# Kernel optimization log

Hardware: AMD Instinct MI355X
Metric: run time of the kernel (lower is better)

The kernel has to match this reference:

```python
import jax, jax.numpy as jnp
import numpy as np
from jax import lax

B, CIN, H, W = 1, 1024, 48, 160
FEAT = 64            # PSM_features
D = 48               # depth_channel = max_disp / downsample_scale
EPS = 1e-5


def _bn(x, g, b, m, v, ndim):
    # eval-mode batchnorm over channel axis 1
    shape = (1, -1) + (1,) * (ndim - 2)
    return (x - m.reshape(shape)) * (g.reshape(shape) * lax.rsqrt(v.reshape(shape) + EPS)) + b.reshape(shape)


def _conv3d(x, w, b):
    y = lax.conv_general_dilated(x, w, (1, 1, 1), 'SAME',
                                 dimension_numbers=('NCDHW', 'OIDHW', 'NCDHW'))
    return y + b[None, :, None, None, None]


def setup_inputs() -> dict:
    key = jax.random.key(0)
    ks = jax.random.split(key, 24)
    f32 = jnp.float32
    inp = {}
    inp['left_features'] = jax.random.normal(ks[0], (B, CIN, H, W), f32)
    inp['right_features'] = jax.random.normal(ks[1], (B, CIN, H, W), f32)
    # 1x1 down_sample conv + BN2d
    inp['ds_w'] = jax.random.normal(ks[2], (FEAT, CIN), f32) * (1.0 / np.sqrt(CIN))
    inp['ds_b'] = jax.random.normal(ks[3], (FEAT,), f32) * 0.01
    inp['bn2_g'] = jax.random.uniform(ks[4], (FEAT,), f32, 0.9, 1.1)
    inp['bn2_b'] = jax.random.normal(ks[5], (FEAT,), f32) * 0.01
    inp['bn2_m'] = jax.random.normal(ks[6], (FEAT,), f32) * 0.01
    inp['bn2_v'] = jax.random.uniform(ks[7], (FEAT,), f32, 0.5, 1.5)
    # conv3d block 1: 2*FEAT -> FEAT, 3x3x3
    inp['c3a_w'] = jax.random.normal(ks[8], (FEAT, 2 * FEAT, 3, 3, 3), f32) * (1.0 / np.sqrt(2 * FEAT * 27))
    inp['c3a_b'] = jax.random.normal(ks[9], (FEAT,), f32) * 0.01
    inp['bn3a_g'] = jax.random.uniform(ks[10], (FEAT,), f32, 0.9, 1.1)
    inp['bn3a_b'] = jax.random.normal(ks[11], (FEAT,), f32) * 0.01
    inp['bn3a_m'] = jax.random.normal(ks[12], (FEAT,), f32) * 0.01
    inp['bn3a_v'] = jax.random.uniform(ks[13], (FEAT,), f32, 0.5, 1.5)
    # conv3d block 2: FEAT -> FEAT, 3x3x3
    inp['c3b_w'] = jax.random.normal(ks[14], (FEAT, FEAT, 3, 3, 3), f32) * (1.0 / np.sqrt(FEAT * 27))
    inp['c3b_b'] = jax.random.normal(ks[15], (FEAT,), f32) * 0.01
    inp['bn3b_g'] = jax.random.uniform(ks[16], (FEAT,), f32, 0.9, 1.1)
    inp['bn3b_b'] = jax.random.normal(ks[17], (FEAT,), f32) * 0.01
    inp['bn3b_m'] = jax.random.normal(ks[18], (FEAT,), f32) * 0.01
    inp['bn3b_v'] = jax.random.uniform(ks[19], (FEAT,), f32, 0.5, 1.5)
    return inp


def reference(left_features, right_features, ds_w, ds_b, bn2_g, bn2_b, bn2_m, bn2_v,
              c3a_w, c3a_b, bn3a_g, bn3a_b, bn3a_m, bn3a_v,
              c3b_w, c3b_b, bn3b_g, bn3b_b, bn3b_m, bn3b_v):
    def down_sample(x):
        y = jnp.einsum('bchw,oc->bohw', x, ds_w) + ds_b[None, :, None, None]
        return jax.nn.relu(_bn(y, bn2_g, bn2_b, bn2_m, bn2_v, 4))

    left = down_sample(left_features)    # [B,FEAT,H,W]
    right = down_sample(right_features)  # [B,FEAT,H,W]

    # Cost volume: for disparity i, left copied at w>=i, right shifted right by i.
    d_idx = jnp.arange(D)[:, None]        # [D,1]
    w_idx = jnp.arange(W)[None, :]        # [1,W]
    mask = (w_idx >= d_idx).astype(left.dtype)          # [D,W]
    cost_left = left[:, :, None, :, :] * mask[None, None, :, None, :]  # [B,F,D,H,W]
    shift = jnp.clip(w_idx - d_idx, 0, W - 1)           # [D,W], right[..., w-i]
    right_g = right[:, :, :, shift]                     # [B,F,H,D,W]
    cost_right = jnp.transpose(right_g, (0, 1, 3, 2, 4)) * mask[None, None, :, None, :]
    cost = jnp.concatenate([cost_left, cost_right], axis=1)  # [B,2F,D,H,W]

    y = jax.nn.relu(_bn(_conv3d(cost, c3a_w, c3a_b), bn3a_g, bn3a_b, bn3a_m, bn3a_v, 5))
    y = jax.nn.relu(_bn(_conv3d(y, c3b_w, c3b_b), bn3b_g, bn3b_b, bn3b_m, bn3b_v, 5))
    return y.reshape(B, -1, H, W)  # [B, FEAT*D, H, W]
```

## Files before the change

### kernel.cpp

```cpp
#include <hip/hip_runtime.h>
#include <hip/hip_bf16.h>

#define CIN   1024
#define FEATN 64
#define HH    48
#define WW    160
#define DDN   48
#define EPSV  1e-5f
#define NTAP  27
#define WSLAB 162

typedef __attribute__((ext_vector_type(8))) short bf16x8;
typedef __attribute__((ext_vector_type(4))) float f32x4;
typedef __attribute__((ext_vector_type(4))) unsigned short u16x4;

static __device__ __forceinline__ unsigned short f2bf(float x) {
    __hip_bfloat16 h = __float2bfloat16(x);
    return *(unsigned short*)&h;
}

__global__ void CostVolume_6201932775918_packw(const float* w3, unsigned short* Wb)
{
    int i = (int)(blockIdx.x * 256 + threadIdx.x);
    if (i >= 64 * NTAP * 128) return;
    int ci  = i & 127;
    int tap = (i >> 7) % NTAP;
    int o   = i / (NTAP * 128);
    Wb[i] = f2bf(w3[o * 3456 + ci * 27 + tap]);
}

__global__ void CostVolume_6201932775918_packw2(const float* w3, unsigned short* Wb2)
{
    int i = (int)(blockIdx.x * 256 + threadIdx.x);
    if (i >= 64 * NTAP * 64) return;
    int ci  = i & 63;
    int tap = (i >> 6) % NTAP;
    int o   = i / (NTAP * 64);
    Wb2[i] = f2bf(w3[o * 1728 + ci * 27 + tap]);
}

__global__ void CostVolume_6201932775918_ds(
    const float* Lf, const float* Rf,
    const float* dsw, const float* dsb,
    const float* g2, const float* b2, const float* m2, const float* v2,
    unsigned short* outL, unsigned short* outR)
{
    const float* in = (blockIdx.y == 0) ? Lf : Rf;
    unsigned short* out = (blockIdx.y == 0) ? outL : outR;
    const int t    = (int)threadIdx.x;
    const int pos0 = (int)blockIdx.x * 64;
    const int oq   = t & 15;
    const int pq   = t >> 4;

    __shared__ float chunk[64 * 64];

    float acc[4][4];
    #pragma unroll
    for (int k = 0; k < 4; ++k)
        #pragma unroll
        for (int j = 0; j < 4; ++j) acc[k][j] = 0.f;

    for (int cc = 0; cc < 16; ++cc) {
        __syncthreads();
        #pragma unroll
        for (int i = 0; i < 16; ++i) {
            int idx = i * 256 + t;
            int cl = idx >> 6;
            int p  = idx & 63;
            chunk[cl * 64 + p] = in[(cc * 64 + cl) * (HH * WW) + pos0 + p];
        }
        __syncthreads();
        for (int cl = 0; cl < 64; ++cl) {
            int c = cc * 64 + cl;
            float x0 = chunk[cl * 64 + pq * 4 + 0];
            float x1 = chunk[cl * 64 + pq * 4 + 1];
            float x2 = chunk[cl * 64 + pq * 4 + 2];
            float x3 = chunk[cl * 64 + pq * 4 + 3];
            #pragma unroll
            for (int k = 0; k < 4; ++k) {
                float w = dsw[(4 * oq + k) * CIN + c];
                acc[k][0] = fmaf(w, x0, acc[k][0]);
                acc[k][1] = fmaf(w, x1, acc[k][1]);
                acc[k][2] = fmaf(w, x2, acc[k][2]);
                acc[k][3] = fmaf(w, x3, acc[k][3]);
            }
        }
    }

    float s4[4], cb4[4];
    #pragma unroll
    for (int k = 0; k < 4; ++k) {
        int o = 4 * oq + k;
        s4[k]  = g2[o] / sqrtf(v2[o] + EPSV);
        cb4[k] = dsb[o] * s4[k] + b2[o] - m2[o] * s4[k];
    }
    #pragma unroll
    for (int j = 0; j < 4; ++j) {
        u16x4 v;
        #pragma unroll
        for (int k = 0; k < 4; ++k)
            v[k] = f2bf(fmaxf(0.f, fmaf(acc[k][j], s4[k], cb4[k])));
        *(u16x4*)&out[(size_t)(pos0 + pq * 4 + j) * 64 + 4 * oq] = v;
    }
}

__global__ __launch_bounds__(256) void CostVolume_6201932775918_c3a(
    const unsigned short* Lt, const unsigned short* Rt,
    const unsigned short* Wb,
    const float* cb3, const float* g3, const float* b3,
    const float* m3, const float* v3,
    unsigned short* y1t)
{
    const int h    = (int)blockIdx.x;
    const int d    = (int)blockIdx.y;
    const int t    = (int)threadIdx.x;
    const int wave = t >> 6;
    const int lane = t & 63;
    const int l15  = lane & 15;
    const int lhi  = lane >> 4;

    __shared__ __align__(16) unsigned short slab[WSLAB * 128];

    f32x4 acc[10];
    #pragma unroll
    for (int n = 0; n < 10; ++n) acc[n] = (f32x4){0.f, 0.f, 0.f, 0.f};

    char* slabB = (char*)slab;
    const int sw0 = t >> 4;

    for (int kd = 0; kd < 3; ++kd) {
        const int dp = d + kd - 1;
        if (dp < 0 || dp >= DDN) continue;
        for (int kh = 0; kh < 3; ++kh) {
            const int hp = h + kh - 1;
            if (hp < 0 || hp >= HH) continue;
            __syncthreads();
            const unsigned short* Lrow = Lt + (size_t)hp * WW * 64;
            const unsigned short* Rrow = Rt + ((size_t)hp * WW - (size_t)dp) * 64;
            #pragma unroll
            for (int i = 0; i < 11; ++i) {
                int e = i * 256 + t;
                if (e < WSLAB * 16) {
                    int wIdx = e >> 4;
                    int c16  = e & 15;
                    int wp   = wIdx - 1;
                    u16x4 v0 = (u16x4){0, 0, 0, 0}, v1 = (u16x4){0, 0, 0, 0};
                    if (wp >= dp && wp < WW) {
                        const unsigned short* src =
                            (c16 < 8) ? (Lrow + (size_t)wp * 64 + c16 * 8)
                                      : (Rrow + (size_t)wp * 64 + (c16 - 8) * 8);
                        v0 = *(const u16x4*)src;
                        v1 = *(const u16x4*)(src + 4);
                    }
                    int byte = (wIdx * 256 + c16 * 16) ^ ((wIdx & 15) << 4);
                    *(u16x4*)(slabB + byte)     = v0;
                    *(u16x4*)(slabB + byte + 8) = v1;
                }
            }
            __syncthreads();
            const int tapbase = (kd * 3 + kh) * 3;
            #pragma unroll
            for (int kw = 0; kw < 3; ++kw) {
                const unsigned short* wrow =
                    Wb + (16 * wave + l15) * (NTAP * 128) + (tapbase + kw) * 128 + lhi * 8;
                #pragma unroll
                for (int kc = 0; kc < 4; ++kc) {
                    bf16x8 afrag = *(const bf16x8*)(wrow + kc * 32);
                    const int ci0x2 = (kc * 32 + lhi * 8) * 2;
                    #pragma unroll
                    for (int n = 0; n < 10; ++n) {
                        int wIdx = 16 * n + l15 + kw;
                        int byte = (wIdx * 256 + ci0x2) ^ ((wIdx & 15) << 4);
                        bf16x8 bfrag = *(const bf16x8*)(slabB + byte);
                        acc[n] = __builtin_amdgcn_mfma_f32_16x16x32_bf16(
                            afrag, bfrag, acc[n], 0, 0, 0);
                    }
                }
            }
        }
    }
    (void)sw0;

    float s4[4], cb4[4];
    #pragma unroll
    for (int r = 0; r < 4; ++r) {
        const int o = 16 * wave + lhi * 4 + r;
        s4[r]  = g3[o] / sqrtf(v3[o] + EPSV);
        cb4[r] = cb3[o] * s4[r] + b3[o] - m3[o] * s4[r];
    }
    unsigned short* ybase =
        y1t + ((size_t)(d * HH + h) * WW) * 64 + 16 * wave + lhi * 4;
    #pragma unroll
    for (int n = 0; n < 10; ++n) {
        int w = 16 * n + l15;
        u16x4 v;
        #pragma unroll
        for (int r = 0; r < 4; ++r)
            v[r] = f2bf(fmaxf(0.f, fmaf(acc[n][r], s4[r], cb4[r])));
        *(u16x4*)(ybase + (size_t)w * 64) = v;
    }
}

__global__ __launch_bounds__(256) void CostVolume_6201932775918_c3b(
    const unsigned short* y1t, const unsigned short* Wb2,
    const float* cb3, const float* g3, const float* b3,
    const float* m3, const float* v3,
    float* outp)
{
    const int h    = (int)blockIdx.x;
    const int d    = (int)blockIdx.y;
    const int t    = (int)threadIdx.x;
    const int wave = t >> 6;
    const int lane = t & 63;
    const int l15  = lane & 15;
    const int lhi  = lane >> 4;

    __shared__ __align__(16) unsigned short slab[WSLAB * 64];

    f32x4 acc[10];
    #pragma unroll
    for (int n = 0; n < 10; ++n) acc[n] = (f32x4){0.f, 0.f, 0.f, 0.f};

    char* slabB = (char*)slab;

    for (int kd = 0; kd < 3; ++kd) {
        const int dp = d + kd - 1;
        if (dp < 0 || dp >= DDN) continue;
        for (int kh = 0; kh < 3; ++kh) {
            const int hp = h + kh - 1;
            if (hp < 0 || hp >= HH) continue;
            __syncthreads();
            const unsigned short* yrow = y1t + ((size_t)(dp * HH + hp) * WW) * 64;
            #pragma unroll
            for (int i = 0; i < 6; ++i) {
                int e = i * 256 + t;
                if (e < WSLAB * 8) {
                    int wIdx = e >> 3;
                    int c16  = e & 7;
                    int wp   = wIdx - 1;
                    u16x4 v0 = (u16x4){0, 0, 0, 0}, v1 = (u16x4){0, 0, 0, 0};
                    if (wp >= 0 && wp < WW) {
                        const unsigned short* src = yrow + (size_t)wp * 64 + c16 * 8;
                        v0 = *(const u16x4*)src;
                        v1 = *(const u16x4*)(src + 4);
                    }
                    int byte = (wIdx * 128 + c16 * 16) ^ ((wIdx & 7) << 4);
                    *(u16x4*)(slabB + byte)     = v0;
                    *(u16x4*)(slabB + byte + 8) = v1;
                }
            }
            __syncthreads();
            const int tapbase = (kd * 3 + kh) * 3;
            #pragma unroll
            for (int kw = 0; kw < 3; ++kw) {
                const unsigned short* wrow =
                    Wb2 + (16 * wave + l15) * (NTAP * 64) + (tapbase + kw) * 64 + lhi * 8;
                #pragma unroll
                for (int kc = 0; kc < 2; ++kc) {
                    bf16x8 afrag = *(const bf16x8*)(wrow + kc * 32);
                    const int ci0x2 = (kc * 32 + lhi * 8) * 2;
                    #pragma unroll
                    for (int n = 0; n < 10; ++n) {
                        int wIdx = 16 * n + l15 + kw;
                        int byte = (wIdx * 128 + ci0x2) ^ ((wIdx & 7) << 4);
                        bf16x8 bfrag = *(const bf16x8*)(slabB + byte);
                        acc[n] = __builtin_amdgcn_mfma_f32_16x16x32_bf16(
                            afrag, bfrag, acc[n], 0, 0, 0);
                    }
                }
            }
        }
    }

    float s4[4], cb4[4];
    #pragma unroll
    for (int r = 0; r < 4; ++r) {
        const int o = 16 * wave + lhi * 4 + r;
        s4[r]  = g3[o] / sqrtf(v3[o] + EPSV);
        cb4[r] = cb3[o] * s4[r] + b3[o] - m3[o] * s4[r];
    }
    #pragma unroll
    for (int r = 0; r < 4; ++r) {
        const int o = 16 * wave + lhi * 4 + r;
        float* orow = outp + ((size_t)(o * DDN + d) * HH + h) * WW;
        #pragma unroll
        for (int n = 0; n < 10; ++n) {
            int w = 16 * n + l15;
            orow[w] = fmaxf(0.f, fmaf(acc[n][r], s4[r], cb4[r]));
        }
    }
}

extern "C" void kernel_launch(void* const* d_in, const int* in_sizes, int n_in,
                              void* d_out, int out_size, void* d_ws, size_t ws_size,
                              hipStream_t stream)
{
    (void)in_sizes; (void)n_in; (void)out_size;

    const float* Lf  = (const float*)d_in[0];
    const float* Rf  = (const float*)d_in[1];
    const float* dsw = (const float*)d_in[2];
    const float* dsb = (const float*)d_in[3];
    const float* g2  = (const float*)d_in[4];
    const float* b2  = (const float*)d_in[5];
    const float* m2  = (const float*)d_in[6];
    const float* v2  = (const float*)d_in[7];
    const float* w3a = (const float*)d_in[8];
    const float* cba = (const float*)d_in[9];
    const float* g3a = (const float*)d_in[10];
    const float* b3a = (const float*)d_in[11];
    const float* m3a = (const float*)d_in[12];
    const float* v3a = (const float*)d_in[13];
    const float* w3b = (const float*)d_in[14];
    const float* cbb = (const float*)d_in[15];
    const float* g3b = (const float*)d_in[16];
    const float* b3b = (const float*)d_in[17];
    const float* m3b = (const float*)d_in[18];
    const float* v3b = (const float*)d_in[19];

    float* outF = (float*)d_out;

    unsigned short* Lt  = (unsigned short*)d_ws;
    unsigned short* Rt  = (unsigned short*)((char*)d_ws + 983040);
    unsigned short* Wb  = (unsigned short*)((char*)d_ws + 1966080);
    unsigned short* Wb2 = (unsigned short*)((char*)d_ws + 2408448);
    unsigned short* y1t = (unsigned short*)((char*)d_ws + 2629632);
    if (ws_size < 2629632 + (size_t)DDN * HH * WW * 64 * 2) return;

    CostVolume_6201932775918_packw<<<dim3(864), 256, 0, stream>>>(w3a, Wb);
    CostVolume_6201932775918_packw2<<<dim3(432), 256, 0, stream>>>(w3b, Wb2);

    CostVolume_6201932775918_ds<<<dim3(120, 2), 256, 0, stream>>>(
        Lf, Rf, dsw, dsb, g2, b2, m2, v2, Lt, Rt);

    CostVolume_6201932775918_c3a<<<dim3(48, 48), 256, 0, stream>>>(
        Lt, Rt, Wb, cba, g3a, b3a, m3a, v3a, y1t);

    CostVolume_6201932775918_c3b<<<dim3(48, 48), 256, 0, stream>>>(
        y1t, Wb2, cbb, g3b, b3b, m3b, v3b, outF);
}
```

Baseline: 477.6 us.

## Reuse left slab across depth taps, double-buffer slabs, skip masked MFMA tiles

In the first 3D conv, the loop order is swapped to kh-outer so the left-feature slab is loaded once per row and reused across the three depth taps. Only the shifted right slab is reloaded, and it is double-buffered, which removes one barrier per tap. MFMA tiles lying entirely in the masked region (w < dp) are skipped, and the left input is zeroed in registers where the mask applies. The second conv also double-buffers its slab and drops the leading barrier, so the load for the next tap can overlap compute on the previous one. The trade-off is more LDS per block and more complex control flow.

New measurement: 490.1 us. 1.03x slower.

```diff
diff --git a/kernel.cpp b/kernel.cpp
--- a/kernel.cpp
+++ b/kernel.cpp
@@ -119,67 +119,88 @@
     const int l15  = lane & 15;
     const int lhi  = lane >> 4;
 
-    __shared__ __align__(16) unsigned short slab[WSLAB * 128];
+    __shared__ __align__(16) unsigned short Lsl[WSLAB * 64];
+    __shared__ __align__(16) unsigned short Rsl[2][WSLAB * 64];
 
     f32x4 acc[10];
     #pragma unroll
     for (int n = 0; n < 10; ++n) acc[n] = (f32x4){0.f, 0.f, 0.f, 0.f};
 
-    char* slabB = (char*)slab;
-    const int sw0 = t >> 4;
-
-    for (int kd = 0; kd < 3; ++kd) {
-        const int dp = d + kd - 1;
-        if (dp < 0 || dp >= DDN) continue;
-        for (int kh = 0; kh < 3; ++kh) {
-            const int hp = h + kh - 1;
-            if (hp < 0 || hp >= HH) continue;
-            __syncthreads();
-            const unsigned short* Lrow = Lt + (size_t)hp * WW * 64;
-            const unsigned short* Rrow = Rt + ((size_t)hp * WW - (size_t)dp) * 64;
-            #pragma unroll
-            for (int i = 0; i < 11; ++i) {
+    char* LB = (char*)Lsl;
+    int buf = 0;
+
+    for (int kh = 0; kh < 3; ++kh) {
+        const int hp = h + kh - 1;
+        if (hp < 0 || hp >= HH) continue;
+        __syncthreads();
+        const unsigned short* Lrow = Lt + (size_t)hp * WW * 64;
+        #pragma unroll
+        for (int i = 0; i < 6; ++i) {
+            int e = i * 256 + t;
+            if (e < WSLAB * 8) {
+                int wIdx = e >> 3, c8 = e & 7, wp = wIdx - 1;
+                u16x4 v0 = (u16x4){0, 0, 0, 0}, v1 = (u16x4){0, 0, 0, 0};
+                if (wp >= 0 && wp < WW) {
+                    const unsigned short* src = Lrow + (size_t)wp * 64 + c8 * 8;
+                    v0 = *(const u16x4*)src;
+                    v1 = *(const u16x4*)(src + 4);
+                }
+                int byte = (wIdx * 128 + c8 * 16) ^ ((wIdx & 7) << 4);
+                *(u16x4*)(LB + byte)     = v0;
+                *(u16x4*)(LB + byte + 8) = v1;
+            }
+        }
+        const unsigned short* Rrow = Rt + (size_t)hp * WW * 64;
+        for (int kd = 0; kd < 3; ++kd) {
+            const int dp = d + kd - 1;
+            if (dp < 0 || dp >= DDN) continue;
+            char* RB = (char*)Rsl[buf];
+            #pragma unroll
+            for (int i = 0; i < 6; ++i) {
                 int e = i * 256 + t;
-                if (e < WSLAB * 16) {
-                    int wIdx = e >> 4;
-                    int c16  = e & 15;
-                    int wp   = wIdx - 1;
+                if (e < WSLAB * 8) {
+                    int wIdx = e >> 3, c8 = e & 7, wp = wIdx - 1;
                     u16x4 v0 = (u16x4){0, 0, 0, 0}, v1 = (u16x4){0, 0, 0, 0};
                     if (wp >= dp && wp < WW) {
                         const unsigned short* src =
-                            (c16 < 8) ? (Lrow + (size_t)wp * 64 + c16 * 8)
-                                      : (Rrow + (size_t)wp * 64 + (c16 - 8) * 8);
+                            Rrow + (size_t)(wp - dp) * 64 + c8 * 8;
                         v0 = *(const u16x4*)src;
                         v1 = *(const u16x4*)(src + 4);
                     }
-                    int byte = (wIdx * 256 + c16 * 16) ^ ((wIdx & 15) << 4);
-                    *(u16x4*)(slabB + byte)     = v0;
-                    *(u16x4*)(slabB + byte + 8) = v1;
+                    int byte = (wIdx * 128 + c8 * 16) ^ ((wIdx & 7) << 4);
+                    *(u16x4*)(RB + byte)     = v0;
+                    *(u16x4*)(RB + byte + 8) = v1;
                 }
             }
             __syncthreads();
-            const int tapbase = (kd * 3 + kh) * 3;
+            const int tap0 = (kd * 3 + kh) * 3;
             #pragma unroll
             for (int kw = 0; kw < 3; ++kw) {
                 const unsigned short* wrow =
-                    Wb + (16 * wave + l15) * (NTAP * 128) + (tapbase + kw) * 128 + lhi * 8;
+                    Wb + (16 * wave + l15) * (NTAP * 128) + (tap0 + kw) * 128 + lhi * 8;
                 #pragma unroll
                 for (int kc = 0; kc < 4; ++kc) {
                     bf16x8 afrag = *(const bf16x8*)(wrow + kc * 32);
-                    const int ci0x2 = (kc * 32 + lhi * 8) * 2;
+                    const bool isL = (kc < 2);
+                    const int ci2 = ((isL ? kc : kc - 2) * 32 + lhi * 8) * 2;
+                    const char* base = isL ? LB : RB;
                     #pragma unroll
                     for (int n = 0; n < 10; ++n) {
-                        int wIdx = 16 * n + l15 + kw;
-                        int byte = (wIdx * 256 + ci0x2) ^ ((wIdx & 15) << 4);
-                        bf16x8 bfrag = *(const bf16x8*)(slabB + byte);
-                        acc[n] = __builtin_amdgcn_mfma_f32_16x16x32_bf16(
-                            afrag, bfrag, acc[n], 0, 0, 0);
+                        if (16 * n + 14 + kw >= dp) {
+                            int wIdx = 16 * n + l15 + kw;
+                            int byte = (wIdx * 128 + ci2) ^ ((wIdx & 7) << 4);
+                            bf16x8 b = *(const bf16x8*)(base + byte);
+                            if (isL && wIdx < dp + 1)
+                                b = (bf16x8){0, 0, 0, 0, 0, 0, 0, 0};
+                            acc[n] = __builtin_amdgcn_mfma_f32_16x16x32_bf16(
+                                afrag, b, acc[n], 0, 0, 0);
+                        }
                     }
                 }
             }
-        }
-    }
-    (void)sw0;
+            buf ^= 1;
+        }
+    }
 
     float s4[4], cb4[4];
     #pragma unroll
@@ -215,13 +236,13 @@
     const int l15  = lane & 15;
     const int lhi  = lane >> 4;
 
-    __shared__ __align__(16) unsigned short slab[WSLAB * 64];
+    __shared__ __align__(16) unsigned short S[2][WSLAB * 64];
 
     f32x4 acc[10];
     #pragma unroll
     for (int n = 0; n < 10; ++n) acc[n] = (f32x4){0.f, 0.f, 0.f, 0.f};
 
-    char* slabB = (char*)slab;
+    int buf = 0;
 
     for (int kd = 0; kd < 3; ++kd) {
         const int dp = d + kd - 1;
@@ -229,46 +250,45 @@
         for (int kh = 0; kh < 3; ++kh) {
             const int hp = h + kh - 1;
             if (hp < 0 || hp >= HH) continue;
-            __syncthreads();
+            char* SB = (char*)S[buf];
             const unsigned short* yrow = y1t + ((size_t)(dp * HH + hp) * WW) * 64;
             #pragma unroll
             for (int i = 0; i < 6; ++i) {
                 int e = i * 256 + t;
                 if (e < WSLAB * 8) {
-                    int wIdx = e >> 3;
-                    int c16  = e & 7;
-                    int wp   = wIdx - 1;
+                    int wIdx = e >> 3, c8 = e & 7, wp = wIdx - 1;
                     u16x4 v0 = (u16x4){0, 0, 0, 0}, v1 = (u16x4){0, 0, 0, 0};
                     if (wp >= 0 && wp < WW) {
-                        const unsigned short* src = yrow + (size_t)wp * 64 + c16 * 8;
+                        const unsigned short* src = yrow + (size_t)wp * 64 + c8 * 8;
                         v0 = *(const u16x4*)src;
                         v1 = *(const u16x4*)(src + 4);
                     }
-                    int byte = (wIdx * 128 + c16 * 16) ^ ((wIdx & 7) << 4);
-                    *(u16x4*)(slabB + byte)     = v0;
-                    *(u16x4*)(slabB + byte + 8) = v1;
+                    int byte = (wIdx * 128 + c8 * 16) ^ ((wIdx & 7) << 4);
+                    *(u16x4*)(SB + byte)     = v0;
+                    *(u16x4*)(SB + byte + 8) = v1;
                 }
             }
             __syncthreads();
-            const int tapbase = (kd * 3 + kh) * 3;
+            const int tap0 = (kd * 3 + kh) * 3;
             #pragma unroll
             for (int kw = 0; kw < 3; ++kw) {
                 const unsigned short* wrow =
-                    Wb2 + (16 * wave + l15) * (NTAP * 64) + (tapbase + kw) * 64 + lhi * 8;
+                    Wb2 + (16 * wave + l15) * (NTAP * 64) + (tap0 + kw) * 64 + lhi * 8;
                 #pragma unroll
                 for (int kc = 0; kc < 2; ++kc) {
                     bf16x8 afrag = *(const bf16x8*)(wrow + kc * 32);
-                    const int ci0x2 = (kc * 32 + lhi * 8) * 2;
+                    const int ci2 = (kc * 32 + lhi * 8) * 2;
                     #pragma unroll
                     for (int n = 0; n < 10; ++n) {
                         int wIdx = 16 * n + l15 + kw;
-                        int byte = (wIdx * 128 + ci0x2) ^ ((wIdx & 7) << 4);
-                        bf16x8 bfrag = *(const bf16x8*)(slabB + byte);
+                        int byte = (wIdx * 128 + ci2) ^ ((wIdx & 7) << 4);
+                        bf16x8 b = *(const bf16x8*)(SB + byte);
                         acc[n] = __builtin_amdgcn_mfma_f32_16x16x32_bf16(
-                            afrag, bfrag, acc[n], 0, 0, 0);
+                            afrag, b, acc[n], 0, 0, 0);
                     }
                 }
             }
+            buf ^= 1;
         }
     }
 
```
